# Optimization experiments

Measured on AMD Instinct MI355X. Metric: run time of the kernel, lower is better.

## Reference

```python
import jax, jax.numpy as jnp
import numpy as np

N, F, H, O, D = 4096, 128, 4, 64, 64


def setup_inputs() -> dict:
    key = jax.random.key(0)
    k1, k2, k3, k4, k5 = jax.random.split(key, 5)
    h = jax.random.normal(k1, (1, N, F), dtype=jnp.float32)
    # dense binary adjacency (0/1)
    a = jax.random.randint(k2, (1, N, N), 0, 2).astype(jnp.float32)
    kernel = jax.random.normal(k3, (H, F, O), dtype=jnp.float32) * 0.1
    attn_kernel = jax.random.normal(k4, (H, F, D), dtype=jnp.float32) * 0.1
    attn_kernel2 = jax.random.normal(k5, (H, F, D), dtype=jnp.float32) * 0.1
    return {"h": h, "a": a, "kernel": kernel, "attn_kernel": attn_kernel, "attn_kernel2": attn_kernel2}


def reference(h, a, kernel, attn_kernel, attn_kernel2):
    x = h[0]          # [N, F]
    adj = a[0]        # [N, N] dense 0/1 adjacency
    # per-head linear projections, vectorized over heads
    feats = jnp.einsum('nf,hfo->hno', x, kernel)          # [H, N, O]
    f_self = jnp.einsum('nf,hfd->hnd', x, attn_kernel)    # [H, N, D]
    f_other = jnp.einsum('nf,hfd->hnd', x, attn_kernel2)  # [H, N, D]
    # dense attention logits, masked BEFORE the nonlinearity (as in original)
    dense = jnp.einsum('hnd,hmd->hnm', f_self, f_other)   # [H, N, N]
    masked = adj[None] * dense
    masked = jnp.where(masked >= 0, masked, 0.2 * masked)  # LeakyReLU(0.2)
    masked = masked / jnp.sqrt(jnp.asarray(D, jnp.float32))
    neg_inf = jnp.where(adj == 0, jnp.float32(-1e9), jnp.float32(0.0))  # [N, N]
    att = jax.nn.softmax(masked + neg_inf[None], axis=-1)
    att = att * (adj != 0).astype(att.dtype)[None]
    # aggregation (dropout is identity at inference, rate=0)
    node_features = jnp.einsum('hnm,hmo->hno', att, feats)  # [H, N, O]
    node_features = jax.nn.relu(node_features)
    # zero out padding rows (all-zero input features)
    row_mask = (jnp.sum((x != 0).astype(jnp.float32), axis=-1, keepdims=True) > 0).astype(jnp.float32)  # [N, 1]
    node_features = node_features * row_mask[None]
    # concat heads along last dim -> [1, N, H*O]
    out = jnp.transpose(node_features, (1, 0, 2)).reshape(N, H * O)
    return out[None]
```

## Files before the change

### kernel.cpp

```cpp
#include <hip/hip_runtime.h>
#include <hip/hip_bf16.h>

typedef unsigned short u16;
typedef unsigned int u32;
typedef unsigned long long u64;
typedef __attribute__((ext_vector_type(8))) short bf16x8;
typedef __attribute__((ext_vector_type(4))) float f32x4;
typedef __attribute__((ext_vector_type(4))) u16 u16x4;

#define N 4096
#define F 128
#define H 4
#define O 64
#define NW (N / 64)
#define NT 8
#define NZ 4
#define QSCALE 0.18033688011112043f

__device__ inline float exp2_hw(float x) {
#if __has_builtin(__builtin_amdgcn_exp2f)
  return __builtin_amdgcn_exp2f(x);
#else
  return __expf(x * 0.6931471805599453f);
#endif
}

__device__ inline u16 f2bf(float f) {
  union { __hip_bfloat16 b; u16 u; } v;
  v.b = __float2bfloat16(f);
  return v.u;
}

__device__ inline float bf2f(u16 u) {
  union { float f; u32 i; } v; v.i = ((u32)u) << 16; return v.f;
}

__global__ __launch_bounds__(256) void prep_kernel(
    const float* __restrict__ x, const float* __restrict__ adj,
    const float* __restrict__ wv, const float* __restrict__ wq,
    const float* __restrict__ wk, u16* __restrict__ Q, u16* __restrict__ K,
    u16* __restrict__ Vt, float* __restrict__ rmask, u64* __restrict__ bits) {
  const int b = blockIdx.x;
  const int t = threadIdx.x;

  if (b < 1024) {
    const int w = t >> 6, l = t & 63;
    const int row = b * 4 + w;
    const float* ar = adj + (size_t)row * N;
    u64* br = bits + (size_t)row * NW;
#pragma unroll 4
    for (int j2 = 0; j2 < 16; j2++) {
      float4 v = *(const float4*)&ar[j2 * 256 + l * 4];
      unsigned nib = (unsigned)(v.x != 0.f) | ((unsigned)(v.y != 0.f) << 1) |
                     ((unsigned)(v.z != 0.f) << 2) | ((unsigned)(v.w != 0.f) << 3);
      u64 word = (u64)nib << ((l & 15) * 4);
      word |= __shfl_xor(word, 1);
      word |= __shfl_xor(word, 2);
      word |= __shfl_xor(word, 4);
      word |= __shfl_xor(word, 8);
      if ((l & 15) == 0) br[j2 * 4 + (l >> 4)] = word;
    }
  } else if (b < 1792) {
    __shared__ __align__(16) u16 xb[64][136];
    __shared__ __align__(16) u16 wt[64][136];
    const int pb = b - 1024;
    const int brow = (pb & 63) * 64;
    const int p = pb >> 6, h = p / 3, which = p % 3;
    const float* W = (which == 0 ? wq : which == 1 ? wk : wv) + h * F * O;

#pragma unroll
    for (int i = 0; i < 8; i++) {
      int idx = t + i * 256, r = idx >> 5, c4 = idx & 31;
      float4 v = *(const float4*)&x[(brow + r) * F + c4 * 4];
      u16x4 o4 = { f2bf(v.x), f2bf(v.y), f2bf(v.z), f2bf(v.w) };
      *(u16x4*)&xb[r][c4 * 4] = o4;
    }
#pragma unroll
    for (int i = 0; i < 8; i++) {
      int idx = t + i * 256, k = idx >> 4, n4 = idx & 15;
      float4 v = *(const float4*)&W[k * O + n4 * 4];
      wt[n4 * 4 + 0][k] = f2bf(v.x);
      wt[n4 * 4 + 1][k] = f2bf(v.y);
      wt[n4 * 4 + 2][k] = f2bf(v.z);
      wt[n4 * 4 + 3][k] = f2bf(v.w);
    }
    __syncthreads();

    const int w = t >> 6, l = t & 63;
    const int lm = l & 15, lg = l >> 4;
    const f32x4 z4 = {0.f, 0.f, 0.f, 0.f};
    bf16x8 af[4];
#pragma unroll
    for (int kc = 0; kc < 4; kc++)
      af[kc] = *(const bf16x8*)&xb[w * 16 + lm][kc * 32 + lg * 8];
    f32x4 acc[4];
#pragma unroll
    for (int ct = 0; ct < 4; ct++) {
      acc[ct] = z4;
#pragma unroll
      for (int kc = 0; kc < 4; kc++) {
        bf16x8 bfr = *(const bf16x8*)&wt[ct * 16 + lm][kc * 32 + lg * 8];
        acc[ct] = __builtin_amdgcn_mfma_f32_16x16x32_bf16(af[kc], bfr, acc[ct], 0, 0, 0);
      }
    }

    const int orow = brow + w * 16 + lg * 4;
    if (which == 0) {
      u16* dst = Q + h * N * O;
#pragma unroll
      for (int ct = 0; ct < 4; ct++)
#pragma unroll
        for (int r = 0; r < 4; r++)
          dst[(orow + r) * O + ct * 16 + lm] = f2bf(acc[ct][r] * QSCALE);
    } else if (which == 1) {
      u16* dst = K + h * N * O;
#pragma unroll
      for (int ct = 0; ct < 4; ct++)
#pragma unroll
        for (int r = 0; r < 4; r++)
          dst[(orow + r) * O + ct * 16 + lm] = f2bf(acc[ct][r]);
    } else {
      u16* dst = Vt + h * O * N;
#pragma unroll
      for (int ct = 0; ct < 4; ct++) {
        u16x4 v4 = { f2bf(acc[ct][0]), f2bf(acc[ct][1]),
                     f2bf(acc[ct][2]), f2bf(acc[ct][3]) };
        *(u16x4*)&dst[(size_t)(ct * 16 + lm) * N + orow] = v4;
      }
    }
  } else {
    int n = (b - 1792) * 256 + t;
    const float4* xr = (const float4*)(x + n * F);
    float s = 0.f;
#pragma unroll
    for (int i = 0; i < F / 4; i++) {
      float4 v = xr[i];
      s += fabsf(v.x) + fabsf(v.y) + fabsf(v.z) + fabsf(v.w);
    }
    rmask[n] = (s != 0.f) ? 1.f : 0.f;
  }
}

__global__ __launch_bounds__(512, 4) void attn_kernel(
    const u64* __restrict__ bits, const u16* __restrict__ Qg,
    const u16* __restrict__ Kg, const u16* __restrict__ Vtg,
    u16* __restrict__ Opart, float* __restrict__ Spart) {
  __shared__ __align__(16) char kv[2][4][8192];
  __shared__ float Ss2[8][32];

  const int tid = threadIdx.x;
  const int w = tid >> 6, l = tid & 63;
  const int lm = l & 15, lg = l >> 4;
  const int rg = w >> 1, hc = w & 1;
  const int h = blockIdx.y;
  const int z = blockIdx.z;
  const int R0 = blockIdx.x * 128;
  const int WR0 = R0 + rg * 32;
  const int CB0 = z * 1024;

  const char* Kb = (const char*)(Kg + h * N * O);
  const char* Vb = (const char*)(Vtg + h * O * N);
  const u64* bblk = bits + (size_t)WR0 * NW;

  const int srow = w * 8 + (l >> 3);
  const int ssw = (((srow & 3) | (((srow >> 3) & 1) << 2)) << 4);
  const int scol = ((l & 7) * 16) ^ ssw;

  const int krow_base = (lm & 3) + 8 * (lm >> 2);
  const int ksw = (lm & 7) << 4;
  const int vsw = (((lm & 3) | (((lm >> 3) & 1) << 2)) << 4);

  const u16* Qh = Qg + h * N * O;
  bf16x8 qa0 = *(const bf16x8*)&Qh[(WR0 + lm) * O + lg * 8];
  bf16x8 qa1 = *(const bf16x8*)&Qh[(WR0 + lm) * O + 32 + lg * 8];
  bf16x8 qb0 = *(const bf16x8*)&Qh[(WR0 + 16 + lm) * O + lg * 8];
  bf16x8 qb1 = *(const bf16x8*)&Qh[(WR0 + 16 + lm) * O + 32 + lg * 8];

  bf16x8 ones;
#pragma unroll
  for (int i = 0; i < 8; i++) ones[i] = (short)0x3F80;

  f32x4 oaccA[4], oaccB[4];
  f32x4 laccA = {0.f, 0.f, 0.f, 0.f}, laccB = {0.f, 0.f, 0.f, 0.f};
#pragma unroll
  for (int i = 0; i < 4; i++) {
    oaccA[i] = (f32x4){0.f, 0.f, 0.f, 0.f};
    oaccB[i] = (f32x4){0.f, 0.f, 0.f, 0.f};
  }
  const f32x4 zero4 = {0.f, 0.f, 0.f, 0.f};

  auto STAGE = [&](int b, int t) {
    __builtin_amdgcn_global_load_lds(
        (const u32*)(Kb + (size_t)(CB0 + 0 * 512 + t * 64 + srow) * 128 + scol),
        (u32*)&kv[b][0][w * 1024], 16, 0, 0);
    __builtin_amdgcn_global_load_lds(
        (const u32*)(Kb + (size_t)(CB0 + 1 * 512 + t * 64 + srow) * 128 + scol),
        (u32*)&kv[b][1][w * 1024], 16, 0, 0);
    __builtin_amdgcn_global_load_lds(
        (const u32*)(Vb + (size_t)srow * (N * 2) + (CB0 + 0 * 512 + t * 64) * 2 + scol),
        (u32*)&kv[b][2][w * 1024], 16, 0, 0);
    __builtin_amdgcn_global_load_lds(
        (const u32*)(Vb + (size_t)srow * (N * 2) + (CB0 + 1 * 512 + t * 64) * 2 + scol),
        (u32*)&kv[b][3][w * 1024], 16, 0, 0);
  };

  STAGE(0, 0);
  __syncthreads();

  int b = 0;
#pragma unroll 1
  for (int t = 0; t < NT; ++t) {
    if (t + 1 < NT) STAGE(b ^ 1, t + 1);

    const int widx = z * 16 + hc * NT + t;

    u64 wordA = bblk[lm * NW + widx];
    u64 wordB = bblk[(16 + lm) * NW + widx];
    u64 wA = wordA >> (8 * lg);
    u64 wB = wordB >> (8 * lg);

    const char* Kt = &kv[b][hc][0];
    f32x4 sA[4], sB[4];
    __builtin_amdgcn_s_setprio(1);
#pragma unroll
    for (int tt = 0; tt < 4; tt++) {
      const int row = krow_base + 4 * (tt & 1) + 32 * (tt >> 1);
      bf16x8 kb0 = *(const bf16x8*)(Kt + row * 128 + ((lg * 16) ^ ksw));
      bf16x8 kb1 = *(const bf16x8*)(Kt + row * 128 + ((lg * 16 + 64) ^ ksw));
      f32x4 t0 = __builtin_amdgcn_mfma_f32_16x16x32_bf16(kb0, qa0, zero4, 0, 0, 0);
      sA[tt] = __builtin_amdgcn_mfma_f32_16x16x32_bf16(kb1, qa1, t0, 0, 0, 0);
      f32x4 t1 = __builtin_amdgcn_mfma_f32_16x16x32_bf16(kb0, qb0, zero4, 0, 0, 0);
      sB[tt] = __builtin_amdgcn_mfma_f32_16x16x32_bf16(kb1, qb1, t1, 0, 0, 0);
    }
    __builtin_amdgcn_s_setprio(0);

    bf16x8 paA0, paA1, paB0, paB1;
    {
      float pv[4][4];
#pragma unroll
      for (int tt = 0; tt < 4; tt++)
#pragma unroll
        for (int r = 0; r < 4; r++) {
          unsigned bit = (unsigned)(wA >> (4 * (tt & 1) + 32 * (tt >> 1) + r)) & 1u;
          float sv = sA[tt][r];
          float lv = fmaxf(sv, 0.2f * sv);
          pv[tt][r] = bit ? exp2_hw(lv) : 0.f;
        }
#pragma unroll
      for (int r = 0; r < 4; r++) {
        paA0[r]     = (short)f2bf(pv[0][r]);
        paA0[4 + r] = (short)f2bf(pv[1][r]);
        paA1[r]     = (short)f2bf(pv[2][r]);
        paA1[4 + r] = (short)f2bf(pv[3][r]);
      }
    }
    {
      float pv[4][4];
#pragma unroll
      for (int tt = 0; tt < 4; tt++)
#pragma unroll
        for (int r = 0; r < 4; r++) {
          unsigned bit = (unsigned)(wB >> (4 * (tt & 1) + 32 * (tt >> 1) + r)) & 1u;
          float sv = sB[tt][r];
          float lv = fmaxf(sv, 0.2f * sv);
          pv[tt][r] = bit ? exp2_hw(lv) : 0.f;
        }
#pragma unroll
      for (int r = 0; r < 4; r++) {
        paB0[r]     = (short)f2bf(pv[0][r]);
        paB0[4 + r] = (short)f2bf(pv[1][r]);
        paB1[r]     = (short)f2bf(pv[2][r]);
        paB1[4 + r] = (short)f2bf(pv[3][r]);
      }
    }

    const char* Vt_ = &kv[b][2 + hc][0];
    __builtin_amdgcn_s_setprio(1);
#pragma unroll
    for (int ot = 0; ot < 4; ot++) {
      const int o = ot * 16 + lm;
      bf16x8 vb0 = *(const bf16x8*)(Vt_ + o * 128 + ((lg * 16) ^ vsw));
      bf16x8 vb1 = *(const bf16x8*)(Vt_ + o * 128 + ((lg * 16 + 64) ^ vsw));
      oaccA[ot] = __builtin_amdgcn_mfma_f32_16x16x32_bf16(vb0, paA0, oaccA[ot], 0, 0, 0);
      oaccA[ot] = __builtin_amdgcn_mfma_f32_16x16x32_bf16(vb1, paA1, oaccA[ot], 0, 0, 0);
      oaccB[ot] = __builtin_amdgcn_mfma_f32_16x16x32_bf16(vb0, paB0, oaccB[ot], 0, 0, 0);
      oaccB[ot] = __builtin_amdgcn_mfma_f32_16x16x32_bf16(vb1, paB1, oaccB[ot], 0, 0, 0);
    }
    laccA = __builtin_amdgcn_mfma_f32_16x16x32_bf16(ones, paA0, laccA, 0, 0, 0);
    laccA = __builtin_amdgcn_mfma_f32_16x16x32_bf16(ones, paA1, laccA, 0, 0, 0);
    laccB = __builtin_amdgcn_mfma_f32_16x16x32_bf16(ones, paB0, laccB, 0, 0, 0);
    laccB = __builtin_amdgcn_mfma_f32_16x16x32_bf16(ones, paB1, laccB, 0, 0, 0);
    __builtin_amdgcn_s_setprio(0);

    __syncthreads();
    b ^= 1;
  }

  float (*Om2)[128][64] = (float (*)[128][64])&kv[0][0][0];
#pragma unroll
  for (int ot = 0; ot < 4; ot++) {
    *(f32x4*)&Om2[hc][rg * 32 + lm][ot * 16 + lg * 4] = oaccA[ot];
    *(f32x4*)&Om2[hc][rg * 32 + 16 + lm][ot * 16 + lg * 4] = oaccB[ot];
  }
  if (lg == 0) {
    Ss2[w][lm] = laccA[0];
    Ss2[w][16 + lm] = laccB[0];
  }
  __syncthreads();

#pragma unroll
  for (int rr = 0; rr < 2; rr++) {
    const int row = rr * 64 + (tid >> 3);
    const int c0 = (tid & 7) * 8;
    const int grow = R0 + row;
    u16* op = &Opart[(((size_t)z * H + h) * N + grow) * O + c0];
    u16x4 v0 = { f2bf(Om2[0][row][c0 + 0] + Om2[1][row][c0 + 0]),
                 f2bf(Om2[0][row][c0 + 1] + Om2[1][row][c0 + 1]),
                 f2bf(Om2[0][row][c0 + 2] + Om2[1][row][c0 + 2]),
                 f2bf(Om2[0][row][c0 + 3] + Om2[1][row][c0 + 3]) };
    u16x4 v1 = { f2bf(Om2[0][row][c0 + 4] + Om2[1][row][c0 + 4]),
                 f2bf(Om2[0][row][c0 + 5] + Om2[1][row][c0 + 5]),
                 f2bf(Om2[0][row][c0 + 6] + Om2[1][row][c0 + 6]),
                 f2bf(Om2[0][row][c0 + 7] + Om2[1][row][c0 + 7]) };
    *(u16x4*)&op[0] = v0;
    *(u16x4*)&op[4] = v1;
    if ((tid & 7) == 0) {
      const int rg2 = row >> 5, ri = row & 31;
      Spart[((size_t)z * H + h) * N + grow] = Ss2[rg2 * 2 + 0][ri] + Ss2[rg2 * 2 + 1][ri];
    }
  }
}

__global__ __launch_bounds__(256) void merge_kernel(
    const u16* __restrict__ Opart, const float* __restrict__ Spart,
    const float* __restrict__ rowmask, float* __restrict__ out) {
  const int h = blockIdx.y;
  const int idx = blockIdx.x * 256 + threadIdx.x;
  const int row = idx >> 4, c0 = (idx & 15) * 4;
  float S = 0.f;
#pragma unroll
  for (int z = 0; z < NZ; z++) S += Spart[((size_t)z * H + h) * N + row];
  float inv = (S > 0.f) ? 1.f / S : 0.f;
  float rm = rowmask[row];
  float a0 = 0.f, a1 = 0.f, a2 = 0.f, a3 = 0.f;
#pragma unroll
  for (int z = 0; z < NZ; z++) {
    u16x4 v = *(const u16x4*)&Opart[(((size_t)z * H + h) * N + row) * O + c0];
    a0 += bf2f(v[0]); a1 += bf2f(v[1]); a2 += bf2f(v[2]); a3 += bf2f(v[3]);
  }
  float4 r;
  r.x = fmaxf(a0 * inv, 0.f) * rm;
  r.y = fmaxf(a1 * inv, 0.f) * rm;
  r.z = fmaxf(a2 * inv, 0.f) * rm;
  r.w = fmaxf(a3 * inv, 0.f) * rm;
  *(float4*)&out[(size_t)row * (H * O) + h * O + c0] = r;
}

extern "C" void kernel_launch(void* const* d_in, const int* in_sizes, int n_in,
                              void* d_out, int out_size, void* d_ws, size_t ws_size,
                              hipStream_t stream) {
  const float* x   = (const float*)d_in[0];
  const float* adj = (const float*)d_in[1];
  const float* wv  = (const float*)d_in[2];
  const float* wq  = (const float*)d_in[3];
  const float* wk  = (const float*)d_in[4];
  float* out = (float*)d_out;

  u16* Q  = (u16*)d_ws;
  u16* K  = Q + H * N * O;
  u16* Vt = K + H * N * O;
  float* rmask = (float*)(Vt + H * N * O);
  u64* bits = (u64*)(rmask + N);
  u16* Opart = (u16*)(bits + (size_t)N * NW);
  float* Spart = (float*)(Opart + (size_t)NZ * H * N * O);

  prep_kernel<<<dim3(1808), 256, 0, stream>>>(x, adj, wv, wq, wk, Q, K, Vt, rmask, bits);
  attn_kernel<<<dim3(N / 128, H, NZ), 512, 0, stream>>>(bits, Q, K, Vt, Opart, Spart);
  merge_kernel<<<dim3(N * O / 4 / 256, H), 256, 0, stream>>>(Opart, Spart, rmask, out);
}
```

Baseline: 66.85 us.

## Fuse split-K merge into attention kernel via last-block atomic counter

Removes the separate merge kernel launch. Each attention block bumps a per-(head,row-tile) atomic counter after writing its partial results, and the last of the NZ blocks to arrive reduces all partials and writes the final output. The counters are reset by an extra block in the prep kernel. The Om2 staging buffer is also padded to 66 columns to reduce LDS bank conflicts, which grows shared memory and may reduce occupancy.

```diff
diff --git a/kernel.cpp b/kernel.cpp
--- a/kernel.cpp
+++ b/kernel.cpp
@@ -39,7 +39,8 @@
     const float* __restrict__ x, const float* __restrict__ adj,
     const float* __restrict__ wv, const float* __restrict__ wq,
     const float* __restrict__ wk, u16* __restrict__ Q, u16* __restrict__ K,
-    u16* __restrict__ Vt, float* __restrict__ rmask, u64* __restrict__ bits) {
+    u16* __restrict__ Vt, float* __restrict__ rmask, u64* __restrict__ bits,
+    int* __restrict__ cnt) {
   const int b = blockIdx.x;
   const int t = threadIdx.x;
 
@@ -128,7 +129,7 @@
         *(u16x4*)&dst[(size_t)(ct * 16 + lm) * N + orow] = v4;
       }
     }
-  } else {
+  } else if (b < 1808) {
     int n = (b - 1792) * 256 + t;
     const float4* xr = (const float4*)(x + n * F);
     float s = 0.f;
@@ -138,15 +139,22 @@
       s += fabsf(v.x) + fabsf(v.y) + fabsf(v.z) + fabsf(v.w);
     }
     rmask[n] = (s != 0.f) ? 1.f : 0.f;
+  } else {
+    if (t < H * (N / 128)) cnt[t] = 0;
   }
 }
 
 __global__ __launch_bounds__(512, 4) void attn_kernel(
     const u64* __restrict__ bits, const u16* __restrict__ Qg,
     const u16* __restrict__ Kg, const u16* __restrict__ Vtg,
-    u16* __restrict__ Opart, float* __restrict__ Spart) {
-  __shared__ __align__(16) char kv[2][4][8192];
+    u16* __restrict__ Opart, float* __restrict__ Spart,
+    const float* __restrict__ rmask, float* __restrict__ out,
+    int* __restrict__ cnt) {
+  __shared__ __align__(16) char smem[67584];
   __shared__ float Ss2[8][32];
+  __shared__ int lastflag;
+
+  char (*kv)[4][8192] = (char (*)[4][8192])&smem[0];
 
   const int tid = threadIdx.x;
   const int w = tid >> 6, l = tid & 63;
@@ -296,7 +304,7 @@
     b ^= 1;
   }
 
-  float (*Om2)[128][64] = (float (*)[128][64])&kv[0][0][0];
+  float (*Om2)[128][66] = (float (*)[128][66])&smem[0];
 #pragma unroll
   for (int ot = 0; ot < 4; ot++) {
     *(f32x4*)&Om2[hc][rg * 32 + lm][ot * 16 + lg * 4] = oaccA[ot];
@@ -329,31 +337,39 @@
       Spart[((size_t)z * H + h) * N + grow] = Ss2[rg2 * 2 + 0][ri] + Ss2[rg2 * 2 + 1][ri];
     }
   }
-}
-
-__global__ __launch_bounds__(256) void merge_kernel(
-    const u16* __restrict__ Opart, const float* __restrict__ Spart,
-    const float* __restrict__ rowmask, float* __restrict__ out) {
-  const int h = blockIdx.y;
-  const int idx = blockIdx.x * 256 + threadIdx.x;
-  const int row = idx >> 4, c0 = (idx & 15) * 4;
-  float S = 0.f;
-#pragma unroll
-  for (int z = 0; z < NZ; z++) S += Spart[((size_t)z * H + h) * N + row];
-  float inv = (S > 0.f) ? 1.f / S : 0.f;
-  float rm = rowmask[row];
-  float a0 = 0.f, a1 = 0.f, a2 = 0.f, a3 = 0.f;
-#pragma unroll
-  for (int z = 0; z < NZ; z++) {
-    u16x4 v = *(const u16x4*)&Opart[(((size_t)z * H + h) * N + row) * O + c0];
-    a0 += bf2f(v[0]); a1 += bf2f(v[1]); a2 += bf2f(v[2]); a3 += bf2f(v[3]);
-  }
-  float4 r;
-  r.x = fmaxf(a0 * inv, 0.f) * rm;
-  r.y = fmaxf(a1 * inv, 0.f) * rm;
-  r.z = fmaxf(a2 * inv, 0.f) * rm;
-  r.w = fmaxf(a3 * inv, 0.f) * rm;
-  *(float4*)&out[(size_t)row * (H * O) + h * O + c0] = r;
+
+  __threadfence();
+  if (tid == 0) {
+    int old = atomicAdd(&cnt[h * (N / 128) + blockIdx.x], 1);
+    lastflag = (old == NZ - 1) ? 1 : 0;
+  }
+  __syncthreads();
+  if (lastflag == 0) return;
+  __threadfence();
+
+#pragma unroll
+  for (int k = 0; k < 4; k++) {
+    const int idx = tid + k * 512;
+    const int row = idx >> 4, c0 = (idx & 15) * 4;
+    const int grow = R0 + row;
+    float S = 0.f;
+#pragma unroll
+    for (int zz = 0; zz < NZ; zz++) S += Spart[((size_t)zz * H + h) * N + grow];
+    float inv = (S > 0.f) ? 1.f / S : 0.f;
+    float rm = rmask[grow];
+    float a0 = 0.f, a1 = 0.f, a2 = 0.f, a3 = 0.f;
+#pragma unroll
+    for (int zz = 0; zz < NZ; zz++) {
+      u16x4 v = *(const u16x4*)&Opart[(((size_t)zz * H + h) * N + grow) * O + c0];
+      a0 += bf2f(v[0]); a1 += bf2f(v[1]); a2 += bf2f(v[2]); a3 += bf2f(v[3]);
+    }
+    float4 r;
+    r.x = fmaxf(a0 * inv, 0.f) * rm;
+    r.y = fmaxf(a1 * inv, 0.f) * rm;
+    r.z = fmaxf(a2 * inv, 0.f) * rm;
+    r.w = fmaxf(a3 * inv, 0.f) * rm;
+    *(float4*)&out[(size_t)grow * (H * O) + h * O + c0] = r;
+  }
 }
 
 extern "C" void kernel_launch(void* const* d_in, const int* in_sizes, int n_in,
@@ -373,8 +389,8 @@
   u64* bits = (u64*)(rmask + N);
   u16* Opart = (u16*)(bits + (size_t)N * NW);
   float* Spart = (float*)(Opart + (size_t)NZ * H * N * O);
-
-  prep_kernel<<<dim3(1808), 256, 0, stream>>>(x, adj, wv, wq, wk, Q, K, Vt, rmask, bits);
-  attn_kernel<<<dim3(N / 128, H, NZ), 512, 0, stream>>>(bits, Q, K, Vt, Opart, Spart);
-  merge_kernel<<<dim3(N * O / 4 / 256, H), 256, 0, stream>>>(Opart, Spart, rmask, out);
-}
+  int* cnt = (int*)(Spart + (size_t)NZ * H * N);
+
+  prep_kernel<<<dim3(1809), 256, 0, stream>>>(x, adj, wv, wq, wk, Q, K, Vt, rmask, bits, cnt);
+  attn_kernel<<<dim3(N / 128, H, NZ), 512, 0, stream>>>(bits, Q, K, Vt, Opart, Spart, rmask, out, cnt);
+}
```

Result: slower. 164.5 us (+146.1%).

## Drop K/V double buffering and shrink epilogue LDS to raise attention occupancy

Applied to the files above, without the earlier changes.

The attention kernel now uses a single K/V staging buffer instead of two, cutting its LDS footprint roughly in half, and raises the launch-bounds occupancy hint from 4 to 8. Each iteration loads its tile and then synchronises before computing, so loads no longer overlap compute. The epilogue reduction is also reworked: one half-wave group writes bf16 partials to a small padded LDS tile and the other adds them from registers and writes the output directly. The aim is more resident blocks per CU, but it gives up prefetch overlap, may force register spills under the tighter per-thread register limit, and rounds one partial sum to bf16 before the add.

```diff
diff --git a/kernel.cpp b/kernel.cpp
--- a/kernel.cpp
+++ b/kernel.cpp
@@ -141,12 +141,14 @@
   }
 }
 
-__global__ __launch_bounds__(512, 4) void attn_kernel(
+__global__ __launch_bounds__(512, 8) void attn_kernel(
     const u64* __restrict__ bits, const u16* __restrict__ Qg,
     const u16* __restrict__ Kg, const u16* __restrict__ Vtg,
     u16* __restrict__ Opart, float* __restrict__ Spart) {
-  __shared__ __align__(16) char kv[2][4][8192];
+  __shared__ __align__(16) char smem[33792];
   __shared__ float Ss2[8][32];
+
+  char (*kv)[8192] = (char (*)[8192])&smem[0];
 
   const int tid = threadIdx.x;
   const int w = tid >> 6, l = tid & 63;
@@ -189,28 +191,25 @@
   }
   const f32x4 zero4 = {0.f, 0.f, 0.f, 0.f};
 
-  auto STAGE = [&](int b, int t) {
+  auto STAGE = [&](int t) {
     __builtin_amdgcn_global_load_lds(
         (const u32*)(Kb + (size_t)(CB0 + 0 * 512 + t * 64 + srow) * 128 + scol),
-        (u32*)&kv[b][0][w * 1024], 16, 0, 0);
+        (u32*)&kv[0][w * 1024], 16, 0, 0);
     __builtin_amdgcn_global_load_lds(
         (const u32*)(Kb + (size_t)(CB0 + 1 * 512 + t * 64 + srow) * 128 + scol),
-        (u32*)&kv[b][1][w * 1024], 16, 0, 0);
+        (u32*)&kv[1][w * 1024], 16, 0, 0);
     __builtin_amdgcn_global_load_lds(
         (const u32*)(Vb + (size_t)srow * (N * 2) + (CB0 + 0 * 512 + t * 64) * 2 + scol),
-        (u32*)&kv[b][2][w * 1024], 16, 0, 0);
+        (u32*)&kv[2][w * 1024], 16, 0, 0);
     __builtin_amdgcn_global_load_lds(
         (const u32*)(Vb + (size_t)srow * (N * 2) + (CB0 + 1 * 512 + t * 64) * 2 + scol),
-        (u32*)&kv[b][3][w * 1024], 16, 0, 0);
+        (u32*)&kv[3][w * 1024], 16, 0, 0);
   };
 
-  STAGE(0, 0);
-  __syncthreads();
-
-  int b = 0;
 #pragma unroll 1
   for (int t = 0; t < NT; ++t) {
-    if (t + 1 < NT) STAGE(b ^ 1, t + 1);
+    STAGE(t);
+    __syncthreads();
 
     const int widx = z * 16 + hc * NT + t;
 
@@ -219,7 +218,7 @@
     u64 wA = wordA >> (8 * lg);
     u64 wB = wordB >> (8 * lg);
 
-    const char* Kt = &kv[b][hc][0];
+    const char* Kt = &kv[hc][0];
     f32x4 sA[4], sB[4];
     __builtin_amdgcn_s_setprio(1);
 #pragma unroll
@@ -274,7 +273,7 @@
       }
     }
 
-    const char* Vt_ = &kv[b][2 + hc][0];
+    const char* Vt_ = &kv[2 + hc][0];
     __builtin_amdgcn_s_setprio(1);
 #pragma unroll
     for (int ot = 0; ot < 4; ot++) {
@@ -293,40 +292,43 @@
     __builtin_amdgcn_s_setprio(0);
 
     __syncthreads();
-    b ^= 1;
-  }
-
-  float (*Om2)[128][64] = (float (*)[128][64])&kv[0][0][0];
-#pragma unroll
-  for (int ot = 0; ot < 4; ot++) {
-    *(f32x4*)&Om2[hc][rg * 32 + lm][ot * 16 + lg * 4] = oaccA[ot];
-    *(f32x4*)&Om2[hc][rg * 32 + 16 + lm][ot * 16 + lg * 4] = oaccB[ot];
-  }
-  if (lg == 0) {
-    Ss2[w][lm] = laccA[0];
-    Ss2[w][16 + lm] = laccB[0];
+  }
+
+  u16 (*OmH)[68] = (u16 (*)[68])&smem[0];
+  if (hc == 1) {
+    const int r0 = rg * 32;
+#pragma unroll
+    for (int ot = 0; ot < 4; ot++) {
+      u16x4 a = { f2bf(oaccA[ot][0]), f2bf(oaccA[ot][1]),
+                  f2bf(oaccA[ot][2]), f2bf(oaccA[ot][3]) };
+      *(u16x4*)&OmH[r0 + lm][ot * 16 + lg * 4] = a;
+      u16x4 bq = { f2bf(oaccB[ot][0]), f2bf(oaccB[ot][1]),
+                   f2bf(oaccB[ot][2]), f2bf(oaccB[ot][3]) };
+      *(u16x4*)&OmH[r0 + 16 + lm][ot * 16 + lg * 4] = bq;
+    }
+    if (lg == 0) {
+      Ss2[w][lm] = laccA[0];
+      Ss2[w][16 + lm] = laccB[0];
+    }
   }
   __syncthreads();
-
-#pragma unroll
-  for (int rr = 0; rr < 2; rr++) {
-    const int row = rr * 64 + (tid >> 3);
-    const int c0 = (tid & 7) * 8;
-    const int grow = R0 + row;
-    u16* op = &Opart[(((size_t)z * H + h) * N + grow) * O + c0];
-    u16x4 v0 = { f2bf(Om2[0][row][c0 + 0] + Om2[1][row][c0 + 0]),
-                 f2bf(Om2[0][row][c0 + 1] + Om2[1][row][c0 + 1]),
-                 f2bf(Om2[0][row][c0 + 2] + Om2[1][row][c0 + 2]),
-                 f2bf(Om2[0][row][c0 + 3] + Om2[1][row][c0 + 3]) };
-    u16x4 v1 = { f2bf(Om2[0][row][c0 + 4] + Om2[1][row][c0 + 4]),
-                 f2bf(Om2[0][row][c0 + 5] + Om2[1][row][c0 + 5]),
-                 f2bf(Om2[0][row][c0 + 6] + Om2[1][row][c0 + 6]),
-                 f2bf(Om2[0][row][c0 + 7] + Om2[1][row][c0 + 7]) };
-    *(u16x4*)&op[0] = v0;
-    *(u16x4*)&op[4] = v1;
-    if ((tid & 7) == 0) {
-      const int rg2 = row >> 5, ri = row & 31;
-      Spart[((size_t)z * H + h) * N + grow] = Ss2[rg2 * 2 + 0][ri] + Ss2[rg2 * 2 + 1][ri];
+  if (hc == 0) {
+    const int r0 = rg * 32;
+    const size_t obase = ((size_t)z * H + h) * N;
+#pragma unroll
+    for (int ot = 0; ot < 4; ot++) {
+      u16x4 hA = *(const u16x4*)&OmH[r0 + lm][ot * 16 + lg * 4];
+      u16x4 hB = *(const u16x4*)&OmH[r0 + 16 + lm][ot * 16 + lg * 4];
+      u16x4 oA = { f2bf(oaccA[ot][0] + bf2f(hA[0])), f2bf(oaccA[ot][1] + bf2f(hA[1])),
+                   f2bf(oaccA[ot][2] + bf2f(hA[2])), f2bf(oaccA[ot][3] + bf2f(hA[3])) };
+      u16x4 oB = { f2bf(oaccB[ot][0] + bf2f(hB[0])), f2bf(oaccB[ot][1] + bf2f(hB[1])),
+                   f2bf(oaccB[ot][2] + bf2f(hB[2])), f2bf(oaccB[ot][3] + bf2f(hB[3])) };
+      *(u16x4*)&Opart[(obase + R0 + r0 + lm) * O + ot * 16 + lg * 4] = oA;
+      *(u16x4*)&Opart[(obase + R0 + r0 + 16 + lm) * O + ot * 16 + lg * 4] = oB;
+    }
+    if (lg == 0) {
+      Spart[obase + R0 + r0 + lm] = laccA[0] + Ss2[w + 1][lm];
+      Spart[obase + R0 + r0 + 16 + lm] = laccB[0] + Ss2[w + 1][16 + lm];
     }
   }
 }
```

New measurement: 185.6 us. 2.78x slower.
